# Kernel optimization log

Measured on AMD Instinct MI355X. Metric: run time of the kernel, lower is better.

The kernel has to match this reference:

```python
import jax, jax.numpy as jnp
import numpy as np

B, C, L = 4, 192, 4096
DIV = 3
CO = C // DIV  # 64


def setup_inputs() -> dict:
    key = jax.random.key(0)
    ks = jax.random.split(key, 6)
    # kaiming-normal-ish init for 1x1 conv weights, stored as (out, in) matrices
    std = float(np.sqrt(2.0 / C))
    return {
        "x": jax.random.normal(ks[0], (B, C, L, 1), dtype=jnp.float32),
        "Wq": jax.random.normal(ks[1], (CO, C), dtype=jnp.float32) * std,
        "Wk": jax.random.normal(ks[2], (CO, C), dtype=jnp.float32) * std,
        "Wv": jax.random.normal(ks[3], (CO, C), dtype=jnp.float32) * std,
        "Wv1": jax.random.normal(ks[4], (CO, C), dtype=jnp.float32) * std,
        "gamma": jnp.zeros((1,), dtype=jnp.float32) + 0.5,  # nonzero so attn path is exercised
    }


def reference(x, Wq, Wk, Wv, Wv1, gamma):
    b, c, l, _ = x.shape
    xf = x.reshape(b, c, l)                      # (B, C, L)
    f = jnp.einsum("oc,bcl->bol", Wq, xf)        # (B, CO, L)
    g = jnp.einsum("oc,bcl->bol", Wk, xf)
    h = jnp.einsum("oc,bcl->bol", Wv, xf)
    v1 = jnp.einsum("oc,bcl->bol", Wv1, xf)
    # scores[b, l, m] = sum_o f[b,o,l] * g[b,o,m]; softmax over dim=1 (l axis)
    scores = jnp.einsum("bol,bom->blm", f, g)    # (B, L, L)
    beta = jax.nn.softmax(scores, axis=1)
    o = gamma * jnp.einsum("bol,blm->bom", h, beta) + v1  # (B, CO, L)
    return o.reshape(b, c // 3, l, 1)
```

## Files before the change

### kernel.cpp

```cpp
#include <hip/hip_runtime.h>
#include <math.h>

#define B_ 4
#define C_ 192
#define L_ 4096
#define CO_ 64
#define LOG2E 1.44269504088896340736f

using half8 = __attribute__((ext_vector_type(8))) _Float16;
using half4v = __attribute__((ext_vector_type(4))) _Float16;
using half2v = __attribute__((ext_vector_type(2))) _Float16;
using f32x16 = __attribute__((ext_vector_type(16))) float;

#if __has_builtin(__builtin_amdgcn_exp2f)
#define EXP2(x) __builtin_amdgcn_exp2f(x)
#else
#define EXP2(x) exp2f(x)
#endif

__device__ inline half2v pkrtz(float a, float b) {
  return __builtin_bit_cast(half2v, __builtin_amdgcn_cvt_pkrtz(a, b));
}


__global__ __launch_bounds__(256) void wpack_kernel(
    const float* __restrict__ Wq, const float* __restrict__ Wk,
    const float* __restrict__ Wv, const float* __restrict__ Wv1,
    _Float16* __restrict__ Wpack) {
  const int tid = blockIdx.x * 256 + threadIdx.x;
  const int w = tid / 1536;
  const int rem = tid % 1536;
  const int og = rem / 768;
  const int ks = (rem % 768) / 64;
  const int lane = rem % 64;
  const float* src = (w == 0) ? Wq : (w == 1) ? Wk : (w == 2) ? Wv : Wv1;
  const float s = (w == 0) ? LOG2E : 1.0f;
  const int row = og * 32 + (lane & 31);
  const int col = ks * 16 + (lane >> 5) * 8;
  const float* p = src + row * C_ + col;
  const float4 a = *(const float4*)(p);
  const float4 c = *(const float4*)(p + 4);
  half8 o;
  half2v t;
  t = pkrtz(a.x * s, a.y * s); o[0] = t[0]; o[1] = t[1];
  t = pkrtz(a.z * s, a.w * s); o[2] = t[0]; o[3] = t[1];
  t = pkrtz(c.x * s, c.y * s); o[4] = t[0]; o[5] = t[1];
  t = pkrtz(c.z * s, c.w * s); o[6] = t[0]; o[7] = t[1];
  *(half8*)(Wpack + (size_t)tid * 8) = o;
}

__global__ __launch_bounds__(256) void proj_mfma(
    const float* __restrict__ x, const _Float16* __restrict__ Wpack,
    _Float16* __restrict__ fPack, _Float16* __restrict__ gPack,
    _Float16* __restrict__ hPack, float* __restrict__ v1N) {
  __shared__ __align__(16) float xs[C_ * 32];
  __shared__ __align__(16) _Float16 fl[32 * 72];
  __shared__ __align__(16) _Float16 gl[32 * 72];
  __shared__ __align__(16) _Float16 hl[64 * 40];
  const int b = blockIdx.y, T = blockIdx.x, l0 = T * 32;
  const int t = threadIdx.x;
  const int lane = t & 63, w = t >> 6;
  const int m = lane & 31, hi = lane >> 5;

  {
    const float* xb = x + (size_t)b * C_ * L_ + l0;
    const int c0 = w * 48;
#pragma unroll
    for (int i = 0; i < 6; ++i) {
      const int cc = c0 + i * 8;
      const float* gp = xb + (size_t)(cc + (lane >> 3)) * L_ + (lane & 7) * 4;
      __builtin_amdgcn_global_load_lds(
          (const __attribute__((address_space(1))) void*)gp,
          (__attribute__((address_space(3))) void*)&xs[cc * 32], 16, 0, 0);
    }
  }

  const _Float16* Wp = Wpack + (size_t)w * 1536 * 8;
  half8 wf[2][12];
#pragma unroll
  for (int og = 0; og < 2; ++og)
#pragma unroll
    for (int ks = 0; ks < 12; ++ks)
      wf[og][ks] =
          *(const half8*)(Wp + ((size_t)(og * 12 + ks) * 64 + lane) * 8);
  __syncthreads();

  if (w < 2) {
    f32x16 acc0 = {}, acc1 = {};
#pragma unroll
    for (int ks = 0; ks < 12; ++ks) {
      const float* xr = &xs[(ks * 16 + hi * 8) * 32 + m];
      half8 aF;
#pragma unroll
      for (int e = 0; e < 8; e += 2) {
        const half2v hp = pkrtz(xr[e * 32], xr[(e + 1) * 32]);
        aF[e] = hp[0]; aF[e + 1] = hp[1];
      }
      acc0 = __builtin_amdgcn_mfma_f32_32x32x16_f16(aF, wf[0][ks], acc0, 0, 0, 0);
      acc1 = __builtin_amdgcn_mfma_f32_32x32x16_f16(aF, wf[1][ks], acc1, 0, 0, 0);
    }
    _Float16* buf = (w == 0) ? fl : gl;
#pragma unroll
    for (int r = 0; r < 16; ++r) {
      const int l = 4 * hi + 8 * (r >> 2) + (r & 3);
      buf[l * 72 + m] = (_Float16)acc0[r];
      buf[l * 72 + 32 + m] = (_Float16)acc1[r];
    }
    _Float16* dst = ((w == 0) ? fPack : gPack) +
                    (size_t)b * L_ * CO_ + (size_t)T * 4 * 64 * 8;
#pragma unroll
    for (int ks = 0; ks < 4; ++ks) {
      const half8 v =
          *(const half8*)&buf[(lane & 31) * 72 + ks * 16 + (lane >> 5) * 8];
      *(half8*)(dst + ((size_t)ks * 64 + lane) * 8) = v;
    }
  } else {
    const int lg = l0 + m;
    for (int oh = 0; oh < 2; ++oh) {
      f32x16 acc = {};
#pragma unroll
      for (int ks = 0; ks < 12; ++ks) {
        const float* xr = &xs[(16 * ks + 8 * hi) * 32 + m];
        half8 bF;
#pragma unroll
        for (int e = 0; e < 8; e += 2) {
          const half2v hp = pkrtz(xr[e * 32], xr[(e + 1) * 32]);
          bF[e] = hp[0]; bF[e + 1] = hp[1];
        }
        acc = __builtin_amdgcn_mfma_f32_32x32x16_f16(wf[oh][ks], bF, acc, 0, 0, 0);
      }
      if (w == 2) {
#pragma unroll
        for (int r = 0; r < 16; ++r) {
          const int o = 32 * oh + 4 * hi + 8 * (r >> 2) + (r & 3);
          hl[o * 40 + m] = (_Float16)acc[r];
        }
      } else {
#pragma unroll
        for (int r = 0; r < 16; ++r) {
          const int o = 32 * oh + 4 * hi + 8 * (r >> 2) + (r & 3);
          v1N[((size_t)b * CO_ + o) * L_ + lg] = acc[r];
        }
      }
    }
    if (w == 2) {
      _Float16* dst = hPack + (size_t)b * L_ * CO_ + (size_t)T * 4 * 64 * 8;
#pragma unroll
      for (int j = 0; j < 4; ++j) {
        const int oh2 = j >> 1, ks2 = j & 1;
        const half8 v = *(const half8*)&hl[(32 * oh2 + (lane & 31)) * 40 +
                                           ks2 * 16 + (lane >> 5) * 8];
        *(half8*)(dst + ((size_t)j * 64 + lane) * 8) = v;
      }
    }
  }
}

__global__ __launch_bounds__(512, 2) void attn_mfma(
    const _Float16* __restrict__ fPack, const _Float16* __restrict__ gPack,
    const _Float16* __restrict__ hPack, const float* __restrict__ v1N,
    const float* __restrict__ gamma_p, float* __restrict__ out) {
  __shared__ __align__(16) _Float16 Pl[8][64 * 40];
  __shared__ float obuf4[4][CO_][65];
  __shared__ float redM[8][64];
  __shared__ float redZ[8][64];

  const int id = blockIdx.x;
  const int b = (id >> 1) & 3;
  const int mt = ((id & 1) << 5) | (id >> 3);
  const int m0 = mt * 64;
  const int t = threadIdx.x;
  const int lane = t & 63, s = t >> 6;
  const int m = lane & 31, hi = lane >> 5;

  const _Float16* fT = fPack + (size_t)b * L_ * CO_;
  const _Float16* hT = hPack + (size_t)b * L_ * CO_;
  _Float16* Pw = &Pl[s][0];

  half8 gf0[4], gf1[4];
  {
    const _Float16* gp = gPack + (size_t)b * L_ * CO_ +
                         (size_t)(2 * mt) * 4 * 64 * 8 + lane * 8;
#pragma unroll
    for (int ks = 0; ks < 4; ++ks) {
      gf0[ks] = *(const half8*)(gp + (size_t)ks * 64 * 8);
      gf1[ks] = *(const half8*)(gp + (size_t)(4 + ks) * 64 * 8);
    }
  }

  f32x16 o0 = {}, o1 = {}, o2 = {}, o3 = {};
  float mx0 = -1e30f, Z0 = 0.f, mx1 = -1e30f, Z1 = 0.f;

  const int T0 = s * 16;
  half8 fc[2][4], hc[2][4];
  {
    const _Float16* fp = fT + ((size_t)T0 * 4 * 64 + lane) * 8;
    const _Float16* hp = hT + ((size_t)T0 * 4 * 64 + lane) * 8;
#pragma unroll
    for (int ks = 0; ks < 4; ++ks) {
      fc[0][ks] = *(const half8*)(fp + (size_t)ks * 64 * 8);
      hc[0][ks] = *(const half8*)(hp + (size_t)ks * 64 * 8);
    }
  }

#pragma unroll 2
  for (int stp = 0; stp < 16; ++stp) {
    const int cur = stp & 1, nxt = cur ^ 1;
    {
      const int Tn = T0 + stp + 1;
      const _Float16* fp = fT + ((size_t)Tn * 4 * 64 + lane) * 8;
      const _Float16* hp = hT + ((size_t)Tn * 4 * 64 + lane) * 8;
#pragma unroll
      for (int ks = 0; ks < 4; ++ks) {
        fc[nxt][ks] = *(const half8*)(fp + (size_t)ks * 64 * 8);
        hc[nxt][ks] = *(const half8*)(hp + (size_t)ks * 64 * 8);
      }
    }
    f32x16 S0 = {}, S1 = {};
#pragma unroll
    for (int ks = 0; ks < 4; ++ks) {
      S0 = __builtin_amdgcn_mfma_f32_32x32x16_f16(fc[cur][ks], gf0[ks], S0, 0, 0, 0);
      S1 = __builtin_amdgcn_mfma_f32_32x32x16_f16(fc[cur][ks], gf1[ks], S1, 0, 0, 0);
    }
    float t0 = S0[0], t1 = S1[0];
#pragma unroll
    for (int r = 1; r < 16; ++r) {
      t0 = fmaxf(t0, S0[r]);
      t1 = fmaxf(t1, S1[r]);
    }
    t0 = fmaxf(t0, __shfl_xor(t0, 32, 64));
    t1 = fmaxf(t1, __shfl_xor(t1, 32, 64));
    if (__any(t0 > mx0 || t1 > mx1)) {
      const float mn0 = fmaxf(mx0, t0), mn1 = fmaxf(mx1, t1);
      const float c0 = EXP2(mx0 - mn0), c1 = EXP2(mx1 - mn1);
      mx0 = mn0; mx1 = mn1;
      Z0 *= c0; Z1 *= c1;
#pragma unroll
      for (int r = 0; r < 16; ++r) {
        o0[r] *= c0; o1[r] *= c0;
        o2[r] *= c1; o3[r] *= c1;
      }
    }
    float zl0 = 0.f, zl1 = 0.f;
#pragma unroll
    for (int u = 0; u < 4; ++u) {
      const float a0 = EXP2(S0[4 * u + 0] - mx0);
      const float a1 = EXP2(S0[4 * u + 1] - mx0);
      const float a2 = EXP2(S0[4 * u + 2] - mx0);
      const float a3 = EXP2(S0[4 * u + 3] - mx0);
      zl0 += (a0 + a1) + (a2 + a3);
      const half2v lo = pkrtz(a0, a1);
      const half2v hi2 = pkrtz(a2, a3);
      half4v w4; w4[0] = lo[0]; w4[1] = lo[1]; w4[2] = hi2[0]; w4[3] = hi2[1];
      *(half4v*)(Pw + m * 40 + 4 * hi + 8 * u) = w4;
      const float b0 = EXP2(S1[4 * u + 0] - mx1);
      const float b1 = EXP2(S1[4 * u + 1] - mx1);
      const float b2 = EXP2(S1[4 * u + 2] - mx1);
      const float b3 = EXP2(S1[4 * u + 3] - mx1);
      zl1 += (b0 + b1) + (b2 + b3);
      const half2v lo2 = pkrtz(b0, b1);
      const half2v hi3 = pkrtz(b2, b3);
      half4v w5; w5[0] = lo2[0]; w5[1] = lo2[1]; w5[2] = hi3[0]; w5[3] = hi3[1];
      *(half4v*)(Pw + (32 + m) * 40 + 4 * hi + 8 * u) = w5;
    }
    Z0 += zl0; Z1 += zl1;
    const half8 bP0 = *(const half8*)(Pw + m * 40 + 8 * hi);
    const half8 bP1 = *(const half8*)(Pw + m * 40 + 16 + 8 * hi);
    const half8 bQ0 = *(const half8*)(Pw + (32 + m) * 40 + 8 * hi);
    const half8 bQ1 = *(const half8*)(Pw + (32 + m) * 40 + 16 + 8 * hi);
    o0 = __builtin_amdgcn_mfma_f32_32x32x16_f16(hc[cur][0], bP0, o0, 0, 0, 0);
    o1 = __builtin_amdgcn_mfma_f32_32x32x16_f16(hc[cur][2], bP0, o1, 0, 0, 0);
    o2 = __builtin_amdgcn_mfma_f32_32x32x16_f16(hc[cur][0], bQ0, o2, 0, 0, 0);
    o3 = __builtin_amdgcn_mfma_f32_32x32x16_f16(hc[cur][2], bQ0, o3, 0, 0, 0);
    o0 = __builtin_amdgcn_mfma_f32_32x32x16_f16(hc[cur][1], bP1, o0, 0, 0, 0);
    o1 = __builtin_amdgcn_mfma_f32_32x32x16_f16(hc[cur][3], bP1, o1, 0, 0, 0);
    o2 = __builtin_amdgcn_mfma_f32_32x32x16_f16(hc[cur][1], bQ1, o2, 0, 0, 0);
    o3 = __builtin_amdgcn_mfma_f32_32x32x16_f16(hc[cur][3], bQ1, o3, 0, 0, 0);
  }

  Z0 += __shfl_xor(Z0, 32, 64);
  Z1 += __shfl_xor(Z1, 32, 64);
  if (hi == 0) {
    redM[s][m] = mx0; redM[s][m + 32] = mx1;
    redZ[s][m] = Z0;  redZ[s][m + 32] = Z1;
  }
  __syncthreads();
  float M0 = redM[0][m], M1 = redM[0][m + 32];
#pragma unroll
  for (int i = 1; i < 8; ++i) {
    M0 = fmaxf(M0, redM[i][m]);
    M1 = fmaxf(M1, redM[i][m + 32]);
  }
  const float sc0 = EXP2(mx0 - M0);
  const float sc1 = EXP2(mx1 - M1);
  if (s < 4) {
#pragma unroll
    for (int r = 0; r < 16; ++r) {
      const int o = 4 * hi + 8 * (r >> 2) + (r & 3);
      obuf4[s][o][m] = sc0 * o0[r];
      obuf4[s][o + 32][m] = sc0 * o1[r];
      obuf4[s][o][m + 32] = sc1 * o2[r];
      obuf4[s][o + 32][m + 32] = sc1 * o3[r];
    }
  }
  __syncthreads();
  if (s >= 4) {
#pragma unroll
    for (int r = 0; r < 16; ++r) {
      const int o = 4 * hi + 8 * (r >> 2) + (r & 3);
      obuf4[s - 4][o][m] += sc0 * o0[r];
      obuf4[s - 4][o + 32][m] += sc0 * o1[r];
      obuf4[s - 4][o][m + 32] += sc1 * o2[r];
      obuf4[s - 4][o + 32][m + 32] += sc1 * o3[r];
    }
  }
  __syncthreads();

  const float gam = gamma_p[0];
  const int me = t & 63;
  const int og = t >> 6;
  float M = redM[0][me];
#pragma unroll
  for (int i = 1; i < 8; ++i) M = fmaxf(M, redM[i][me]);
  float Zt = 0.f;
#pragma unroll
  for (int i = 0; i < 8; ++i) Zt += EXP2(redM[i][me] - M) * redZ[i][me];
  const float inv = 1.0f / Zt;
#pragma unroll
  for (int i = 0; i < 8; ++i) {
    const int o = og * 8 + i;
    const float val = obuf4[0][o][me] + obuf4[1][o][me] +
                      obuf4[2][o][me] + obuf4[3][o][me];
    const size_t g = ((size_t)b * CO_ + o) * L_ + m0 + me;
    out[g] = gam * val * inv + v1N[g];
  }
}

extern "C" void kernel_launch(void* const* d_in, const int* in_sizes, int n_in,
                              void* d_out, int out_size, void* d_ws,
                              size_t ws_size, hipStream_t stream) {
  const float* x = (const float*)d_in[0];
  const float* Wq = (const float*)d_in[1];
  const float* Wk = (const float*)d_in[2];
  const float* Wv = (const float*)d_in[3];
  const float* Wv1 = (const float*)d_in[4];
  const float* gamma = (const float*)d_in[5];
  float* out = (float*)d_out;

  _Float16* Wpack = (_Float16*)d_ws;
  _Float16* fPack = Wpack + (size_t)4 * 1536 * 8;
  _Float16* gPack = fPack + (size_t)B_ * L_ * CO_;
  _Float16* hPack = gPack + (size_t)B_ * L_ * CO_;
  float* v1N = (float*)(hPack + (size_t)B_ * L_ * CO_);

  wpack_kernel<<<24, 256, 0, stream>>>(Wq, Wk, Wv, Wv1, Wpack);
  proj_mfma<<<dim3(L_ / 32, B_), 256, 0, stream>>>(x, Wpack, fPack, gPack,
                                                   hPack, v1N);
  attn_mfma<<<256, 512, 0, stream>>>(fPack, gPack, hPack, v1N, gamma, out);
}
```

Measured before the change: 105.8 us.

## Software-pipeline QK^T MFMA one step ahead and transpose x to fp16 in projection

In the attention kernel, the score MFMAs for the next key tile are issued before the softmax of the current tile, with f prefetched two steps ahead and h loaded per step. The goal is to overlap MFMA latency with the exp and LDS work. The projection kernel now stages x as a transposed fp16 tile in LDS so all warps share one A-fragment layout, and v1 stores are staged through LDS for coalescing. The cost is extra registers for the double-buffered score accumulators, which could hurt occupancy or cause spills under launch_bounds(512,2). The f prefetch also reads two tiles past each segment's range.

```diff
diff --git a/kernel.cpp b/kernel.cpp
--- a/kernel.cpp
+++ b/kernel.cpp
@@ -53,27 +53,16 @@
     const float* __restrict__ x, const _Float16* __restrict__ Wpack,
     _Float16* __restrict__ fPack, _Float16* __restrict__ gPack,
     _Float16* __restrict__ hPack, float* __restrict__ v1N) {
-  __shared__ __align__(16) float xs[C_ * 32];
+  __shared__ __align__(16) _Float16 xT[32][200];
   __shared__ __align__(16) _Float16 fl[32 * 72];
   __shared__ __align__(16) _Float16 gl[32 * 72];
   __shared__ __align__(16) _Float16 hl[64 * 40];
+  __shared__ float vl[64][33];
   const int b = blockIdx.y, T = blockIdx.x, l0 = T * 32;
   const int t = threadIdx.x;
   const int lane = t & 63, w = t >> 6;
   const int m = lane & 31, hi = lane >> 5;
-
-  {
-    const float* xb = x + (size_t)b * C_ * L_ + l0;
-    const int c0 = w * 48;
-#pragma unroll
-    for (int i = 0; i < 6; ++i) {
-      const int cc = c0 + i * 8;
-      const float* gp = xb + (size_t)(cc + (lane >> 3)) * L_ + (lane & 7) * 4;
-      __builtin_amdgcn_global_load_lds(
-          (const __attribute__((address_space(1))) void*)gp,
-          (__attribute__((address_space(3))) void*)&xs[cc * 32], 16, 0, 0);
-    }
-  }
+  const int lr = lane & 31, rp = lane >> 5;
 
   const _Float16* Wp = Wpack + (size_t)w * 1536 * 8;
   half8 wf[2][12];
@@ -83,22 +72,31 @@
     for (int ks = 0; ks < 12; ++ks)
       wf[og][ks] =
           *(const half8*)(Wp + ((size_t)(og * 12 + ks) * 64 + lane) * 8);
+
+  {
+    const float* xb = x + (size_t)b * C_ * L_ + l0 + lr;
+    const int c0 = w * 48;
+#pragma unroll
+    for (int i = 0; i < 24; ++i) {
+      const int c = c0 + 2 * i + rp;
+      xT[lr][c] = (_Float16)xb[(size_t)c * L_];
+    }
+  }
   __syncthreads();
 
+  half8 aF[12];
+#pragma unroll
+  for (int ks = 0; ks < 12; ++ks)
+    aF[ks] = *(const half8*)&xT[m][ks * 16 + hi * 8];
+
+  f32x16 acc0 = {}, acc1 = {};
+#pragma unroll
+  for (int ks = 0; ks < 12; ++ks) {
+    acc0 = __builtin_amdgcn_mfma_f32_32x32x16_f16(aF[ks], wf[0][ks], acc0, 0, 0, 0);
+    acc1 = __builtin_amdgcn_mfma_f32_32x32x16_f16(aF[ks], wf[1][ks], acc1, 0, 0, 0);
+  }
+
   if (w < 2) {
-    f32x16 acc0 = {}, acc1 = {};
-#pragma unroll
-    for (int ks = 0; ks < 12; ++ks) {
-      const float* xr = &xs[(ks * 16 + hi * 8) * 32 + m];
-      half8 aF;
-#pragma unroll
-      for (int e = 0; e < 8; e += 2) {
-        const half2v hp = pkrtz(xr[e * 32], xr[(e + 1) * 32]);
-        aF[e] = hp[0]; aF[e + 1] = hp[1];
-      }
-      acc0 = __builtin_amdgcn_mfma_f32_32x32x16_f16(aF, wf[0][ks], acc0, 0, 0, 0);
-      acc1 = __builtin_amdgcn_mfma_f32_32x32x16_f16(aF, wf[1][ks], acc1, 0, 0, 0);
-    }
     _Float16* buf = (w == 0) ? fl : gl;
 #pragma unroll
     for (int r = 0; r < 16; ++r) {
@@ -114,44 +112,32 @@
           *(const half8*)&buf[(lane & 31) * 72 + ks * 16 + (lane >> 5) * 8];
       *(half8*)(dst + ((size_t)ks * 64 + lane) * 8) = v;
     }
+  } else if (w == 2) {
+#pragma unroll
+    for (int r = 0; r < 16; ++r) {
+      const int l = 4 * hi + 8 * (r >> 2) + (r & 3);
+      hl[m * 40 + l] = (_Float16)acc0[r];
+      hl[(32 + m) * 40 + l] = (_Float16)acc1[r];
+    }
+    _Float16* dst = hPack + (size_t)b * L_ * CO_ + (size_t)T * 4 * 64 * 8;
+#pragma unroll
+    for (int j = 0; j < 4; ++j) {
+      const int oh2 = j >> 1, ks2 = j & 1;
+      const half8 v = *(const half8*)&hl[(32 * oh2 + (lane & 31)) * 40 +
+                                         ks2 * 16 + (lane >> 5) * 8];
+      *(half8*)(dst + ((size_t)j * 64 + lane) * 8) = v;
+    }
   } else {
-    const int lg = l0 + m;
-    for (int oh = 0; oh < 2; ++oh) {
-      f32x16 acc = {};
-#pragma unroll
-      for (int ks = 0; ks < 12; ++ks) {
-        const float* xr = &xs[(16 * ks + 8 * hi) * 32 + m];
-        half8 bF;
-#pragma unroll
-        for (int e = 0; e < 8; e += 2) {
-          const half2v hp = pkrtz(xr[e * 32], xr[(e + 1) * 32]);
-          bF[e] = hp[0]; bF[e + 1] = hp[1];
-        }
-        acc = __builtin_amdgcn_mfma_f32_32x32x16_f16(wf[oh][ks], bF, acc, 0, 0, 0);
-      }
-      if (w == 2) {
-#pragma unroll
-        for (int r = 0; r < 16; ++r) {
-          const int o = 32 * oh + 4 * hi + 8 * (r >> 2) + (r & 3);
-          hl[o * 40 + m] = (_Float16)acc[r];
-        }
-      } else {
-#pragma unroll
-        for (int r = 0; r < 16; ++r) {
-          const int o = 32 * oh + 4 * hi + 8 * (r >> 2) + (r & 3);
-          v1N[((size_t)b * CO_ + o) * L_ + lg] = acc[r];
-        }
-      }
-    }
-    if (w == 2) {
-      _Float16* dst = hPack + (size_t)b * L_ * CO_ + (size_t)T * 4 * 64 * 8;
-#pragma unroll
-      for (int j = 0; j < 4; ++j) {
-        const int oh2 = j >> 1, ks2 = j & 1;
-        const half8 v = *(const half8*)&hl[(32 * oh2 + (lane & 31)) * 40 +
-                                           ks2 * 16 + (lane >> 5) * 8];
-        *(half8*)(dst + ((size_t)j * 64 + lane) * 8) = v;
-      }
+#pragma unroll
+    for (int r = 0; r < 16; ++r) {
+      const int l = 4 * hi + 8 * (r >> 2) + (r & 3);
+      vl[m][l] = acc0[r];
+      vl[32 + m][l] = acc1[r];
+    }
+#pragma unroll
+    for (int i = 0; i < 32; ++i) {
+      const int o = 2 * i + rp;
+      v1N[((size_t)b * CO_ + o) * L_ + l0 + lr] = vl[o][lr];
     }
   }
 }
@@ -192,36 +178,53 @@
   float mx0 = -1e30f, Z0 = 0.f, mx1 = -1e30f, Z1 = 0.f;
 
   const int T0 = s * 16;
-  half8 fc[2][4], hc[2][4];
+  half8 fc[2][4];
+  f32x16 Sv0[2], Sv1[2];
+
   {
     const _Float16* fp = fT + ((size_t)T0 * 4 * 64 + lane) * 8;
-    const _Float16* hp = hT + ((size_t)T0 * 4 * 64 + lane) * 8;
+#pragma unroll
+    for (int ks = 0; ks < 4; ++ks)
+      fc[0][ks] = *(const half8*)(fp + (size_t)ks * 64 * 8);
+    f32x16 z = {};
+    Sv0[0] = z; Sv1[0] = z;
 #pragma unroll
     for (int ks = 0; ks < 4; ++ks) {
-      fc[0][ks] = *(const half8*)(fp + (size_t)ks * 64 * 8);
-      hc[0][ks] = *(const half8*)(hp + (size_t)ks * 64 * 8);
-    }
+      Sv0[0] = __builtin_amdgcn_mfma_f32_32x32x16_f16(fc[0][ks], gf0[ks], Sv0[0], 0, 0, 0);
+      Sv1[0] = __builtin_amdgcn_mfma_f32_32x32x16_f16(fc[0][ks], gf1[ks], Sv1[0], 0, 0, 0);
+    }
+    const _Float16* fp1 = fT + ((size_t)(T0 + 1) * 4 * 64 + lane) * 8;
+#pragma unroll
+    for (int ks = 0; ks < 4; ++ks)
+      fc[1][ks] = *(const half8*)(fp1 + (size_t)ks * 64 * 8);
   }
 
 #pragma unroll 2
   for (int stp = 0; stp < 16; ++stp) {
     const int cur = stp & 1, nxt = cur ^ 1;
+    half8 hc[4];
     {
-      const int Tn = T0 + stp + 1;
-      const _Float16* fp = fT + ((size_t)Tn * 4 * 64 + lane) * 8;
-      const _Float16* hp = hT + ((size_t)Tn * 4 * 64 + lane) * 8;
+      const _Float16* hp = hT + ((size_t)(T0 + stp) * 4 * 64 + lane) * 8;
+#pragma unroll
+      for (int ks = 0; ks < 4; ++ks)
+        hc[ks] = *(const half8*)(hp + (size_t)ks * 64 * 8);
+    }
+    {
+      f32x16 z = {};
+      Sv0[nxt] = z; Sv1[nxt] = z;
 #pragma unroll
       for (int ks = 0; ks < 4; ++ks) {
-        fc[nxt][ks] = *(const half8*)(fp + (size_t)ks * 64 * 8);
-        hc[nxt][ks] = *(const half8*)(hp + (size_t)ks * 64 * 8);
+        Sv0[nxt] = __builtin_amdgcn_mfma_f32_32x32x16_f16(fc[nxt][ks], gf0[ks], Sv0[nxt], 0, 0, 0);
+        Sv1[nxt] = __builtin_amdgcn_mfma_f32_32x32x16_f16(fc[nxt][ks], gf1[ks], Sv1[nxt], 0, 0, 0);
       }
     }
-    f32x16 S0 = {}, S1 = {};
-#pragma unroll
-    for (int ks = 0; ks < 4; ++ks) {
-      S0 = __builtin_amdgcn_mfma_f32_32x32x16_f16(fc[cur][ks], gf0[ks], S0, 0, 0, 0);
-      S1 = __builtin_amdgcn_mfma_f32_32x32x16_f16(fc[cur][ks], gf1[ks], S1, 0, 0, 0);
-    }
+    {
+      const _Float16* fp = fT + ((size_t)(T0 + stp + 2) * 4 * 64 + lane) * 8;
+#pragma unroll
+      for (int ks = 0; ks < 4; ++ks)
+        fc[cur][ks] = *(const half8*)(fp + (size_t)ks * 64 * 8);
+    }
+    const f32x16 S0 = Sv0[cur], S1 = Sv1[cur];
     float t0 = S0[0], t1 = S1[0];
 #pragma unroll
     for (int r = 1; r < 16; ++r) {
@@ -268,14 +271,14 @@
     const half8 bP1 = *(const half8*)(Pw + m * 40 + 16 + 8 * hi);
     const half8 bQ0 = *(const half8*)(Pw + (32 + m) * 40 + 8 * hi);
     const half8 bQ1 = *(const half8*)(Pw + (32 + m) * 40 + 16 + 8 * hi);
-    o0 = __builtin_amdgcn_mfma_f32_32x32x16_f16(hc[cur][0], bP0, o0, 0, 0, 0);
-    o1 = __builtin_amdgcn_mfma_f32_32x32x16_f16(hc[cur][2], bP0, o1, 0, 0, 0);
-    o2 = __builtin_amdgcn_mfma_f32_32x32x16_f16(hc[cur][0], bQ0, o2, 0, 0, 0);
-    o3 = __builtin_amdgcn_mfma_f32_32x32x16_f16(hc[cur][2], bQ0, o3, 0, 0, 0);
-    o0 = __builtin_amdgcn_mfma_f32_32x32x16_f16(hc[cur][1], bP1, o0, 0, 0, 0);
-    o1 = __builtin_amdgcn_mfma_f32_32x32x16_f16(hc[cur][3], bP1, o1, 0, 0, 0);
-    o2 = __builtin_amdgcn_mfma_f32_32x32x16_f16(hc[cur][1], bQ1, o2, 0, 0, 0);
-    o3 = __builtin_amdgcn_mfma_f32_32x32x16_f16(hc[cur][3], bQ1, o3, 0, 0, 0);
+    o0 = __builtin_amdgcn_mfma_f32_32x32x16_f16(hc[0], bP0, o0, 0, 0, 0);
+    o1 = __builtin_amdgcn_mfma_f32_32x32x16_f16(hc[2], bP0, o1, 0, 0, 0);
+    o2 = __builtin_amdgcn_mfma_f32_32x32x16_f16(hc[0], bQ0, o2, 0, 0, 0);
+    o3 = __builtin_amdgcn_mfma_f32_32x32x16_f16(hc[2], bQ0, o3, 0, 0, 0);
+    o0 = __builtin_amdgcn_mfma_f32_32x32x16_f16(hc[1], bP1, o0, 0, 0, 0);
+    o1 = __builtin_amdgcn_mfma_f32_32x32x16_f16(hc[3], bP1, o1, 0, 0, 0);
+    o2 = __builtin_amdgcn_mfma_f32_32x32x16_f16(hc[1], bQ1, o2, 0, 0, 0);
+    o3 = __builtin_amdgcn_mfma_f32_32x32x16_f16(hc[3], bQ1, o3, 0, 0, 0);
   }
 
   Z0 += __shfl_xor(Z0, 32, 64);
```

Result: no change. 105.1 us (-0.6%).
